# Optimization experiments

Hardware: AMD Instinct MI355X
Metric: run time of the kernel (lower is better)

## Reference

```python
import jax, jax.numpy as jnp
import numpy as np

B, D_MODEL, L = 4, 1024, 2048
HEAD_DIM = 4
H = D_MODEL // HEAD_DIM  # 256 heads of size head_dim
KD, NS, INIT_SCALE = 64, 6, 0
DECAY_MIN, DECAY_MAX = 2.0, 2.0


def _interp_linear(x, scale):
    # x: (h, Lin) -> (h, Lin*scale); matches F.interpolate(mode='linear', align_corners=False)
    if scale == 1:
        return x
    Lin = x.shape[-1]
    Lout = Lin * scale
    pos = (jnp.arange(Lout, dtype=jnp.float32) + 0.5) / scale - 0.5
    pos = jnp.clip(pos, 0.0, Lin - 1)
    lo = jnp.floor(pos).astype(jnp.int32)
    hi = jnp.minimum(lo + 1, Lin - 1)
    w = (pos - lo).astype(x.dtype)
    return x[:, lo] * (1 - w) + x[:, hi] * w


def _build_kernel(kernels, L):
    # 'cat_randn' mode: concat multi-scale interpolated kernels with decay multiplier.
    # kernels: (NS, h, KD) -> (h, L), unit-normalized per channel (norm is stop-grad,
    # mirroring the detached kernel_norm buffer initialized on first forward).
    h = kernels.shape[1]
    mult = jnp.linspace(DECAY_MIN, DECAY_MAX, h).astype(kernels.dtype)[:, None]  # (h,1)
    parts = [_interp_linear(kernels[i], 2 ** (max(0, i - 1) + INIT_SCALE)) * mult ** (NS - i - 1)
             for i in range(NS)]
    k = jnp.concatenate(parts, axis=-1)  # (h, KD*2^(NS-1))
    norm = jax.lax.stop_gradient(jnp.linalg.norm(k, axis=-1, keepdims=True))
    Lk = k.shape[-1]
    k = k[:, :L] if Lk >= L else jnp.pad(k, ((0, 0), (0, L - Lk)))
    return k / norm


def setup_inputs() -> dict:
    key = jax.random.key(0)
    ks = jax.random.split(key, 13)
    s = 0.02  # weight init scale
    return {
        'u': jax.random.normal(ks[0], (B, D_MODEL, L), jnp.float32),
        'q_w': jax.random.normal(ks[1], (D_MODEL, D_MODEL), jnp.float32) * s,
        'q_b': jax.random.normal(ks[2], (D_MODEL,), jnp.float32) * s,
        'k_w': jax.random.normal(ks[3], (D_MODEL, D_MODEL), jnp.float32) * s,
        'k_b': jax.random.normal(ks[4], (D_MODEL,), jnp.float32) * s,
        'v_w': jax.random.normal(ks[5], (D_MODEL, D_MODEL), jnp.float32) * s,
        'v_b': jax.random.normal(ks[6], (D_MODEL,), jnp.float32) * s,
        'kernels_key': jax.random.normal(ks[7], (NS, D_MODEL, KD), jnp.float32),
        'kernels': jax.random.normal(ks[8], (NS, H, KD), jnp.float32),
        'D_key': jax.random.normal(ks[9], (1, D_MODEL), jnp.float32),
        'D': jax.random.normal(ks[10], (1, H), jnp.float32),
        'pw_w': jax.random.normal(ks[11], (D_MODEL, D_MODEL), jnp.float32) * s,
        'pw_b': jax.random.normal(ks[12], (D_MODEL,), jnp.float32) * s,
    }


def reference(u, q_w, q_b, k_w, k_b, v_w, v_b, kernels_key, kernels, D_key, D, pw_w, pw_b):
    Bb, Dm, Ll = u.shape
    d = HEAD_DIM
    h = Dm // d
    n = 2 * Ll  # fft size

    k_key = _build_kernel(kernels_key, Ll)  # (Dm, L)
    k_v = _build_kernel(kernels, Ll)        # (h, L)

    # q/k/v projections (W @ u + b along channel dim)
    q = jnp.einsum('oh,bhl->bol', q_w, u) + q_b[None, :, None]
    kk = jnp.einsum('oh,bhl->bol', k_w, u) + k_b[None, :, None]
    v = jnp.einsum('oh,bhl->bol', v_w, u) + v_b[None, :, None]

    # key-side FFT long convolution + skip D_key
    key_conv = jnp.fft.irfft(jnp.fft.rfft(kk, n) * jnp.fft.rfft(k_key, n)[None], n)[..., :Ll]
    kk = key_conv + kk * D_key[0][None, :, None]

    # outer-product gating kv: (B, d1, d2, h, L)
    k_heads = kk.reshape(Bb, h, d, Ll).transpose(0, 2, 1, 3)  # (B, d1, h, L)
    v_heads = v.reshape(Bb, h, d, Ll).transpose(0, 2, 1, 3)   # (B, d2, h, L)
    kv = k_heads[:, :, None] * v_heads[:, None]               # (B, d1, d2, h, L)

    # value-side FFT long convolution + skip D
    y = jnp.fft.irfft(jnp.fft.rfft(kv, n) * jnp.fft.rfft(k_v, n)[None, None, None], n)[..., :Ll]
    y = y + kv * D[0][:, None]

    # query gating: mul_sum over d1
    q_heads = q.reshape(Bb, h, d, Ll).transpose(0, 2, 1, 3)[:, :, None]  # (B, d1, 1, h, L)
    y = (q_heads * y).sum(axis=1)                                        # (B, d2, h, L)
    y = y.reshape(Bb, Dm, Ll)

    # activation + pointwise projection, back to (B, H, L)
    y = jax.nn.gelu(jnp.transpose(y, (0, 2, 1)), approximate=False)
    y = y @ pw_w.T + pw_b
    return jnp.transpose(y, (0, 2, 1))
```

## Files before the change

### kernel.cpp

```cpp
#include <hip/hip_runtime.h>
#include <cmath>

#define B_  4
#define DM  1024
#define LL  2048
#define HH  256

#define KBSTRIDE 2120

typedef short bf16x8 __attribute__((ext_vector_type(8)));
typedef float f32x4 __attribute__((ext_vector_type(4)));

__device__ __forceinline__ float gelu_exact(float x) {
    return x * 0.5f * (1.0f + erff(x * 0.70710678118654752f));
}
__device__ __forceinline__ unsigned short f2b(float f) {
    unsigned int x = __float_as_uint(f);
    unsigned int r = x + 0x7FFFu + ((x >> 16) & 1u);
    return (unsigned short)(r >> 16);
}
__device__ __forceinline__ float b2f(unsigned short u) {
    return __uint_as_float(((unsigned int)u) << 16);
}
__device__ __forceinline__ int cvt_pk_bf16(float lo, float hi) {
    int r;
    asm("v_cvt_pk_bf16_f32 %0, %1, %2" : "=v"(r) : "v"(lo), "v"(hi));
    return r;
}

__global__ __launch_bounds__(256) void build_kernels_kernel(
        const float* __restrict__ src_key,
        const float* __restrict__ src_v,
        unsigned short* __restrict__ k_key,
        float* __restrict__ k_v) {
    int bid = blockIdx.x;
    const float* src;
    int chanstride;
    bool is_key = bid < DM;
    if (is_key) {
        src = src_key + (size_t)bid * 64;
        chanstride = DM * 64;
    } else {
        src = src_v + (size_t)(bid - DM) * 64;
        chanstride = HH * 64;
    }
    int t = threadIdx.x;
    float vals[8];
    float ss = 0.0f;
#pragma unroll
    for (int r = 0; r < 8; ++r) {
        int j = r * 256 + t;
        int i, start, scale;
        if (j < 64)        { i = 0; start = 0;    scale = 1;  }
        else if (j < 128)  { i = 1; start = 64;   scale = 1;  }
        else if (j < 256)  { i = 2; start = 128;  scale = 2;  }
        else if (j < 512)  { i = 3; start = 256;  scale = 4;  }
        else if (j < 1024) { i = 4; start = 512;  scale = 8;  }
        else               { i = 5; start = 1024; scale = 16; }
        int jj = j - start;
        float pos = ((float)jj + 0.5f) / (float)scale - 0.5f;
        pos = fminf(fmaxf(pos, 0.0f), 63.0f);
        int lo = (int)pos;
        int hi = min(lo + 1, 63);
        float w = pos - (float)lo;
        const float* s = src + (size_t)i * chanstride;
        float x0 = s[lo], x1 = s[hi];
        float mult = (float)(1 << (5 - i));
        float vv = (x0 * (1.0f - w) + x1 * w) * mult;
        vals[r] = vv;
        ss += vv * vv;
    }
#pragma unroll
    for (int off = 32; off > 0; off >>= 1) ss += __shfl_down(ss, off, 64);
    __shared__ float red[4];
    __shared__ float norm_s;
    if ((t & 63) == 0) red[t >> 6] = ss;
    __syncthreads();
    if (t == 0) norm_s = sqrtf(red[0] + red[1] + red[2] + red[3]);
    __syncthreads();
    float nrm = norm_s;
    if (is_key) {
        unsigned short* dst = k_key + (size_t)bid * LL;
#pragma unroll
        for (int r = 0; r < 8; ++r) dst[r * 256 + t] = f2b(vals[r] / nrm);
    } else {
        float* dst = k_v + (size_t)(bid - DM) * LL;
#pragma unroll
        for (int r = 0; r < 8; ++r) dst[r * 256 + t] = vals[r] / nrm;
    }
}

__global__ __launch_bounds__(256) void wcvt_kernel(
        const float* __restrict__ src, unsigned short* __restrict__ dst) {
    int i = (blockIdx.x * 256 + threadIdx.x) * 4;
    float4 x = *(const float4*)(src + i);
    ushort4 o;
    o.x = f2b(x.x); o.y = f2b(x.y); o.z = f2b(x.z); o.w = f2b(x.w);
    *(ushort4*)(dst + i) = o;
}

__global__ __launch_bounds__(256) void transpose_cvt_kernel(
        const float* __restrict__ src, unsigned short* __restrict__ dst,
        int do_gelu) {
    __shared__ float tile[64][65];
    int l0 = blockIdx.x << 6;
    int h0 = blockIdx.y << 6;
    int b  = blockIdx.z;
    int t = threadIdx.x;
    int r = t >> 4, c4 = (t & 15) << 2;
    const float* s = src + ((size_t)b * DM + h0) * LL + l0;
#pragma unroll
    for (int p = 0; p < 4; ++p) {
        float4 x = *(const float4*)(s + (size_t)(p * 16 + r) * LL + c4);
        tile[p * 16 + r][c4 + 0] = x.x;
        tile[p * 16 + r][c4 + 1] = x.y;
        tile[p * 16 + r][c4 + 2] = x.z;
        tile[p * 16 + r][c4 + 3] = x.w;
    }
    __syncthreads();
    unsigned short* d = dst + ((size_t)b * LL + l0) * DM + h0;
#pragma unroll
    for (int p = 0; p < 4; ++p) {
        int lr = p * 16 + r;
        float x0 = tile[c4 + 0][lr];
        float x1 = tile[c4 + 1][lr];
        float x2 = tile[c4 + 2][lr];
        float x3 = tile[c4 + 3][lr];
        if (do_gelu) {
            x0 = gelu_exact(x0); x1 = gelu_exact(x1);
            x2 = gelu_exact(x2); x3 = gelu_exact(x3);
        }
        ushort4 o;
        o.x = f2b(x0); o.y = f2b(x1); o.z = f2b(x2); o.w = f2b(x3);
        *(ushort4*)(d + (size_t)lr * DM + c4) = o;
    }
}

__global__ __launch_bounds__(256) void gemm_mfma_kernel(
        const unsigned short* __restrict__ A,
        const unsigned short* __restrict__ Ubf,
        const float* __restrict__ bias,
        float* __restrict__ C) {
    __shared__ unsigned short As[128 * 64];
    __shared__ unsigned short Bs[128 * 64];
    int bidx = blockIdx.x;
    int b = bidx >> 4;
    int n0 = (bidx & 15) << 7;
    int m0 = blockIdx.y << 7;
    int t = threadIdx.x;
    int lane = t & 63, wave = t >> 6;
    int wr = wave >> 1, wc = wave & 1;

    const unsigned short* Ub = Ubf + (size_t)b * LL * DM;

    f32x4 acc[4][4];
#pragma unroll
    for (int i = 0; i < 4; ++i)
#pragma unroll
        for (int j = 0; j < 4; ++j) {
            f32x4 z = {0.0f, 0.0f, 0.0f, 0.0f};
            acc[i][j] = z;
        }

    int srow = t >> 3;
    int scol = (t & 7) << 3;
    int lrow = lane & 15;
    int lk = (lane >> 4) << 3;

    for (int k0 = 0; k0 < DM; k0 += 64) {
        __syncthreads();
#pragma unroll
        for (int p = 0; p < 4; ++p) {
            int row = p * 32 + srow;
            uint4 av = *(const uint4*)(A  + (size_t)(m0 + row) * DM + k0 + scol);
            uint4 bv = *(const uint4*)(Ub + (size_t)(n0 + row) * DM + k0 + scol);
            *(uint4*)&As[row * 64 + scol] = av;
            *(uint4*)&Bs[row * 64 + scol] = bv;
        }
        __syncthreads();
#pragma unroll
        for (int kk = 0; kk < 64; kk += 32) {
            bf16x8 af[4], bfr[4];
#pragma unroll
            for (int mi = 0; mi < 4; ++mi)
                af[mi] = *(const bf16x8*)&As[(wr * 64 + mi * 16 + lrow) * 64 + kk + lk];
#pragma unroll
            for (int ni = 0; ni < 4; ++ni)
                bfr[ni] = *(const bf16x8*)&Bs[(wc * 64 + ni * 16 + lrow) * 64 + kk + lk];
#pragma unroll
            for (int mi = 0; mi < 4; ++mi)
#pragma unroll
                for (int ni = 0; ni < 4; ++ni)
                    acc[mi][ni] = __builtin_amdgcn_mfma_f32_16x16x32_bf16(
                        af[mi], bfr[ni], acc[mi][ni], 0, 0, 0);
        }
    }
    int rg = (lane >> 4) << 2;
    int cn = lane & 15;
#pragma unroll
    for (int mi = 0; mi < 4; ++mi) {
#pragma unroll
        for (int r = 0; r < 4; ++r) {
            int o = m0 + wr * 64 + mi * 16 + rg + r;
            float bo = bias[o];
            float* crow = C + ((size_t)b * DM + o) * LL + n0 + wc * 64;
#pragma unroll
            for (int ni = 0; ni < 4; ++ni)
                crow[ni * 16 + cn] = acc[mi][ni][r] + bo;
        }
    }
}

__global__ __launch_bounds__(512) void key_conv_mfma_kernel(
        const float* __restrict__ kk_raw,
        const unsigned short* __restrict__ k_key,
        const float* __restrict__ D_key,
        float* __restrict__ knew) {
    __shared__ unsigned short Kb[8 * KBSTRIDE];
    int c = blockIdx.x;
    int tid = threadIdx.x;

    const unsigned short* kp = k_key + (size_t)c * LL;
#pragma unroll
    for (int r = 0; r < 8; ++r) {
        for (int x = tid; x < 2096; x += 512) {
            int src = x + r - 48;
            Kb[r * KBSTRIDE + x] =
                (src >= 0 && src < LL) ? kp[src] : (unsigned short)0;
        }
    }
    __syncthreads();

    int w = tid >> 6, lane = tid & 63;
    int n = lane & 15, kgrp = lane >> 4;
    float zmask = (n < 4) ? 1.0f : 0.0f;
    int brow = (n < 4) ? n : 0;
    const float* pk = kk_raw + ((size_t)brow * DM + c) * LL;

    f32x4 acc[16];
#pragma unroll
    for (int m = 0; m < 16; ++m) {
        f32x4 z = {0.0f, 0.0f, 0.0f, 0.0f};
        acc[m] = z;
    }

    int idx0 = 16 * w + n + 8 * kgrp - 1999;
    int rsh = (n + 1) & 7;
    int lbase = rsh * KBSTRIDE + (idx0 - rsh);

    for (int s = 0; s < 64; ++s) {
        int t0p = s << 5;
        int tb = 2040 - t0p - 8 * kgrp;
        float4 ka = *(const float4*)(pk + tb);
        float4 kb = *(const float4*)(pk + tb + 4);
        float p0 = kb.w * zmask;
        float p1 = kb.z * zmask;
        float p2 = kb.y * zmask;
        float p3 = kb.x * zmask;
        float p4 = ka.w * zmask;
        float p5 = ka.z * zmask;
        float p6 = ka.y * zmask;
        float p7 = ka.x * zmask;
        int4 ai;
        ai.x = cvt_pk_bf16(p0, p1);
        ai.y = cvt_pk_bf16(p2, p3);
        ai.z = cvt_pk_bf16(p4, p5);
        ai.w = cvt_pk_bf16(p6, p7);
        bf16x8 afrag = __builtin_bit_cast(bf16x8, ai);

        int msv = (2128 - t0p - 16 * w) >> 7;
        msv = msv < 0 ? 0 : msv;
        int ms = __builtin_amdgcn_readfirstlane(msv);
        const unsigned short* kbp = &Kb[lbase + t0p];

#pragma unroll
        for (int m = 0; m < 16; ++m) {
            if (m >= ms) {
                bf16x8 bfrag = *(const bf16x8*)(kbp + (m << 7));
                acc[m] = __builtin_amdgcn_mfma_f32_16x16x32_bf16(
                    afrag, bfrag, acc[m], 0, 0, 0);
            }
        }
    }

    int g = lane >> 4;
    if (g == 0) {
        float dk = D_key[c];
#pragma unroll
        for (int m = 0; m < 16; ++m) {
            int lm = 16 * w + 128 * m + n;
#pragma unroll
            for (int b = 0; b < 4; ++b) {
                size_t off = ((size_t)b * DM + c) * LL + lm;
                knew[off] = acc[m][b] + kk_raw[off] * dk;
            }
        }
    }
}

__global__ __launch_bounds__(512) void value_conv_mfma_kernel(
        const float* __restrict__ knew,
        const float* __restrict__ v,
        const float* __restrict__ q,
        const float* __restrict__ k_v,
        const float* __restrict__ Dv,
        float* __restrict__ y_g) {
    __shared__ unsigned short Kb[8 * KBSTRIDE];
    int bid = blockIdx.x;
    int hh = bid & 255, b = bid >> 8;
    int tid = threadIdx.x;

    const float* kvp = k_v + (size_t)hh * LL;
#pragma unroll
    for (int r = 0; r < 8; ++r) {
        for (int x = tid; x < 2096; x += 512) {
            int src = x + r - 48;
            Kb[r * KBSTRIDE + x] =
                (src >= 0 && src < LL) ? f2b(kvp[src]) : (unsigned short)0;
        }
    }
    __syncthreads();

    int w = tid >> 6, lane = tid & 63;
    int n = lane & 15, kgrp = lane >> 4;
    int d1a = n >> 2, d2a = n & 3;

    const float* pk = knew + ((size_t)b * DM + hh * 4 + d1a) * LL;
    const float* pv = v    + ((size_t)b * DM + hh * 4 + d2a) * LL;

    f32x4 acc[16];
#pragma unroll
    for (int m = 0; m < 16; ++m) {
        f32x4 z = {0.0f, 0.0f, 0.0f, 0.0f};
        acc[m] = z;
    }

    int idx0 = 16 * w + n + 8 * kgrp - 1999;
    int rsh = (n + 1) & 7;
    int lbase = rsh * KBSTRIDE + (idx0 - rsh);

    for (int s = 0; s < 64; ++s) {
        int t0p = s << 5;
        int tb = 2040 - t0p - 8 * kgrp;
        float4 ka = *(const float4*)(pk + tb);
        float4 kb = *(const float4*)(pk + tb + 4);
        float4 va = *(const float4*)(pv + tb);
        float4 vb = *(const float4*)(pv + tb + 4);
        float p0 = kb.w * vb.w;
        float p1 = kb.z * vb.z;
        float p2 = kb.y * vb.y;
        float p3 = kb.x * vb.x;
        float p4 = ka.w * va.w;
        float p5 = ka.z * va.z;
        float p6 = ka.y * va.y;
        float p7 = ka.x * va.x;
        int4 ai;
        ai.x = cvt_pk_bf16(p0, p1);
        ai.y = cvt_pk_bf16(p2, p3);
        ai.z = cvt_pk_bf16(p4, p5);
        ai.w = cvt_pk_bf16(p6, p7);
        bf16x8 afrag = __builtin_bit_cast(bf16x8, ai);

        int msv = (2128 - t0p - 16 * w) >> 7;
        msv = msv < 0 ? 0 : msv;
        int ms = __builtin_amdgcn_readfirstlane(msv);
        const unsigned short* kbp = &Kb[lbase + t0p];

#pragma unroll
        for (int m = 0; m < 16; ++m) {
            if (m >= ms) {
                bf16x8 bfrag = *(const bf16x8*)(kbp + (m << 7));
                acc[m] = __builtin_amdgcn_mfma_f32_16x16x32_bf16(
                    afrag, bfrag, acc[m], 0, 0, 0);
            }
        }
    }

    int g = lane >> 4;
    float Dh = Dv[hh];
    const float* qrow = q    + ((size_t)b * DM + hh * 4 + g) * LL;
    const float* krow = knew + ((size_t)b * DM + hh * 4 + g) * LL;
    const float* vb0  = v    + ((size_t)b * DM + hh * 4) * LL;
#pragma unroll
    for (int m = 0; m < 16; ++m) {
        int lm = 16 * w + 128 * m + n;
        float qv = qrow[lm];
        float kl = krow[lm];
        float vl0 = vb0[lm];
        float vl1 = vb0[(size_t)1 * LL + lm];
        float vl2 = vb0[(size_t)2 * LL + lm];
        float vl3 = vb0[(size_t)3 * LL + lm];
        float part0 = qv * (acc[m][0] + kl * vl0 * Dh);
        float part1 = qv * (acc[m][1] + kl * vl1 * Dh);
        float part2 = qv * (acc[m][2] + kl * vl2 * Dh);
        float part3 = qv * (acc[m][3] + kl * vl3 * Dh);
        part0 += __shfl_xor(part0, 16, 64); part0 += __shfl_xor(part0, 32, 64);
        part1 += __shfl_xor(part1, 16, 64); part1 += __shfl_xor(part1, 32, 64);
        part2 += __shfl_xor(part2, 16, 64); part2 += __shfl_xor(part2, 32, 64);
        part3 += __shfl_xor(part3, 16, 64); part3 += __shfl_xor(part3, 32, 64);
        float outv = (g == 0) ? part0 : (g == 1) ? part1 : (g == 2) ? part2 : part3;
        y_g[((size_t)b * DM + (size_t)g * 256 + hh) * LL + lm] = outv;
    }
}

extern "C" void kernel_launch(void* const* d_in, const int* in_sizes, int n_in,
                              void* d_out, int out_size, void* d_ws, size_t ws_size,
                              hipStream_t stream) {
    const float* u       = (const float*)d_in[0];
    const float* q_w     = (const float*)d_in[1];
    const float* q_b     = (const float*)d_in[2];
    const float* k_w     = (const float*)d_in[3];
    const float* k_b     = (const float*)d_in[4];
    const float* v_w     = (const float*)d_in[5];
    const float* v_b     = (const float*)d_in[6];
    const float* kern_k  = (const float*)d_in[7];
    const float* kern_v  = (const float*)d_in[8];
    const float* D_key   = (const float*)d_in[9];
    const float* D_v     = (const float*)d_in[10];
    const float* pw_w    = (const float*)d_in[11];
    const float* pw_b    = (const float*)d_in[12];
    float* out = (float*)d_out;

    const size_t BDL = (size_t)B_ * DM * LL;
    char* p = (char*)d_ws;
    float*          w_kv   = (float*)p;          p += (size_t)HH * LL * 4;
    unsigned short* w_kkey = (unsigned short*)p; p += (size_t)DM * LL * 2;
    unsigned short* w_wbuf = (unsigned short*)p; p += (size_t)DM * DM * 2;
    float*          w_R0   = (float*)p;          p += BDL * 4;
    float*          w_q    = (float*)p;          p += BDL * 4;
    float*          w_ky   = (float*)p;          p += BDL * 4;
    float*          w_v    = (float*)p;          p += BDL * 4;
    unsigned short* w_uT   = (unsigned short*)w_R0;
    unsigned short* w_ygT  = (unsigned short*)w_R0;
    float*          w_knew = w_R0;
    float*          w_yg   = w_ky;

    build_kernels_kernel<<<DM + HH, 256, 0, stream>>>(kern_k, kern_v, w_kkey, w_kv);

    dim3 tgrid(LL / 64, DM / 64, B_);
    transpose_cvt_kernel<<<tgrid, 256, 0, stream>>>(u, w_uT, 0);

    dim3 ggrid(B_ * (LL / 128), DM / 128);
    wcvt_kernel<<<DM * DM / 1024, 256, 0, stream>>>(q_w, w_wbuf);
    gemm_mfma_kernel<<<ggrid, 256, 0, stream>>>(w_wbuf, w_uT, q_b, w_q);
    wcvt_kernel<<<DM * DM / 1024, 256, 0, stream>>>(k_w, w_wbuf);
    gemm_mfma_kernel<<<ggrid, 256, 0, stream>>>(w_wbuf, w_uT, k_b, w_ky);
    wcvt_kernel<<<DM * DM / 1024, 256, 0, stream>>>(v_w, w_wbuf);
    gemm_mfma_kernel<<<ggrid, 256, 0, stream>>>(w_wbuf, w_uT, v_b, w_v);

    key_conv_mfma_kernel<<<DM, 512, 0, stream>>>(w_ky, w_kkey, D_key, w_knew);

    value_conv_mfma_kernel<<<B_ * HH, 512, 0, stream>>>(
        w_knew, w_v, w_q, w_kv, D_v, w_yg);

    transpose_cvt_kernel<<<tgrid, 256, 0, stream>>>(w_yg, w_ygT, 1);

    wcvt_kernel<<<DM * DM / 1024, 256, 0, stream>>>(pw_w, w_wbuf);
    gemm_mfma_kernel<<<ggrid, 256, 0, stream>>>(w_wbuf, w_ygT, pw_b, out);
}
```

Before: 567.4 us.

## Reuse Toeplitz B fragments in registers across conv steps via rotating buffer

The causal-convolution MFMA loops in both conv kernels are reordered into four residue classes of the step index. Within each class, consecutive steps share 15 of their 16 shared-memory B fragments, so a 16-entry register ring buffer is filled once and then advanced by one LDS load per step instead of sixteen. Launch bounds are raised to request 2 blocks per CU. This cuts LDS read traffic, but the 16 extra bf16x8 registers on top of the 64 accumulator floats raise register pressure, which conflicts with the occupancy hint and may cause spills.

```diff
diff --git a/kernel.cpp b/kernel.cpp
--- a/kernel.cpp
+++ b/kernel.cpp
@@ -211,7 +211,7 @@
     }
 }
 
-__global__ __launch_bounds__(512) void key_conv_mfma_kernel(
+__global__ __launch_bounds__(512, 2) void key_conv_mfma_kernel(
         const float* __restrict__ kk_raw,
         const unsigned short* __restrict__ k_key,
         const float* __restrict__ D_key,
@@ -246,39 +246,55 @@
 
     int idx0 = 16 * w + n + 8 * kgrp - 1999;
     int rsh = (n + 1) & 7;
-    int lbase = rsh * KBSTRIDE + (idx0 - rsh);
-
-    for (int s = 0; s < 64; ++s) {
-        int t0p = s << 5;
-        int tb = 2040 - t0p - 8 * kgrp;
-        float4 ka = *(const float4*)(pk + tb);
-        float4 kb = *(const float4*)(pk + tb + 4);
-        float p0 = kb.w * zmask;
-        float p1 = kb.z * zmask;
-        float p2 = kb.y * zmask;
-        float p3 = kb.x * zmask;
-        float p4 = ka.w * zmask;
-        float p5 = ka.z * zmask;
-        float p6 = ka.y * zmask;
-        float p7 = ka.x * zmask;
-        int4 ai;
-        ai.x = cvt_pk_bf16(p0, p1);
-        ai.y = cvt_pk_bf16(p2, p3);
-        ai.z = cvt_pk_bf16(p4, p5);
-        ai.w = cvt_pk_bf16(p6, p7);
-        bf16x8 afrag = __builtin_bit_cast(bf16x8, ai);
-
-        int msv = (2128 - t0p - 16 * w) >> 7;
-        msv = msv < 0 ? 0 : msv;
-        int ms = __builtin_amdgcn_readfirstlane(msv);
-        const unsigned short* kbp = &Kb[lbase + t0p];
-
-#pragma unroll
-        for (int m = 0; m < 16; ++m) {
-            if (m >= ms) {
-                bf16x8 bfrag = *(const bf16x8*)(kbp + (m << 7));
-                acc[m] = __builtin_amdgcn_mfma_f32_16x16x32_bf16(
-                    afrag, bfrag, acc[m], 0, 0, 0);
+    const unsigned short* kbp = &Kb[rsh * KBSTRIDE];
+    int aoff0 = idx0 - rsh;
+
+    bf16x8 Bv[16];
+    for (int r = 0; r < 4; ++r) {
+        int off0 = aoff0 + (r << 5);
+#pragma unroll
+        for (int i = 0; i < 15; ++i) {
+            int off = off0 + (i << 7);
+            off = off < 0 ? 0 : off;
+            Bv[i] = *(const bf16x8*)(kbp + off);
+        }
+#pragma unroll
+        for (int si = 0; si < 16; ++si) {
+            {
+                int off = off0 + ((si + 15) << 7);
+                off = off < 0 ? 0 : off;
+                Bv[(si + 15) & 15] = *(const bf16x8*)(kbp + off);
+            }
+            int s = r + (si << 2);
+            int msv = (2128 - (s << 5) - 16 * w) >> 7;
+            msv = msv < 0 ? 0 : msv;
+            int ms = __builtin_amdgcn_readfirstlane(msv);
+            if (ms >= 16) continue;
+
+            int tb = 2040 - (s << 5) - 8 * kgrp;
+            float4 ka = *(const float4*)(pk + tb);
+            float4 kb = *(const float4*)(pk + tb + 4);
+            float p0 = kb.w * zmask;
+            float p1 = kb.z * zmask;
+            float p2 = kb.y * zmask;
+            float p3 = kb.x * zmask;
+            float p4 = ka.w * zmask;
+            float p5 = ka.z * zmask;
+            float p6 = ka.y * zmask;
+            float p7 = ka.x * zmask;
+            int4 ai;
+            ai.x = cvt_pk_bf16(p0, p1);
+            ai.y = cvt_pk_bf16(p2, p3);
+            ai.z = cvt_pk_bf16(p4, p5);
+            ai.w = cvt_pk_bf16(p6, p7);
+            bf16x8 afrag = __builtin_bit_cast(bf16x8, ai);
+
+#pragma unroll
+            for (int m = 0; m < 16; ++m) {
+                if (m >= ms) {
+                    acc[m] = __builtin_amdgcn_mfma_f32_16x16x32_bf16(
+                        afrag, Bv[(si + m) & 15], acc[m], 0, 0, 0);
+                }
             }
         }
     }
@@ -298,7 +314,7 @@
     }
 }
 
-__global__ __launch_bounds__(512) void value_conv_mfma_kernel(
+__global__ __launch_bounds__(512, 2) void value_conv_mfma_kernel(
         const float* __restrict__ knew,
         const float* __restrict__ v,
         const float* __restrict__ q,
@@ -337,41 +353,57 @@
 
     int idx0 = 16 * w + n + 8 * kgrp - 1999;
     int rsh = (n + 1) & 7;
-    int lbase = rsh * KBSTRIDE + (idx0 - rsh);
-
-    for (int s = 0; s < 64; ++s) {
-        int t0p = s << 5;
-        int tb = 2040 - t0p - 8 * kgrp;
-        float4 ka = *(const float4*)(pk + tb);
-        float4 kb = *(const float4*)(pk + tb + 4);
-        float4 va = *(const float4*)(pv + tb);
-        float4 vb = *(const float4*)(pv + tb + 4);
-        float p0 = kb.w * vb.w;
-        float p1 = kb.z * vb.z;
-        float p2 = kb.y * vb.y;
-        float p3 = kb.x * vb.x;
-        float p4 = ka.w * va.w;
-        float p5 = ka.z * va.z;
-        float p6 = ka.y * va.y;
-        float p7 = ka.x * va.x;
-        int4 ai;
-        ai.x = cvt_pk_bf16(p0, p1);
-        ai.y = cvt_pk_bf16(p2, p3);
-        ai.z = cvt_pk_bf16(p4, p5);
-        ai.w = cvt_pk_bf16(p6, p7);
-        bf16x8 afrag = __builtin_bit_cast(bf16x8, ai);
-
-        int msv = (2128 - t0p - 16 * w) >> 7;
-        msv = msv < 0 ? 0 : msv;
-        int ms = __builtin_amdgcn_readfirstlane(msv);
-        const unsigned short* kbp = &Kb[lbase + t0p];
-
-#pragma unroll
-        for (int m = 0; m < 16; ++m) {
-            if (m >= ms) {
-                bf16x8 bfrag = *(const bf16x8*)(kbp + (m << 7));
-                acc[m] = __builtin_amdgcn_mfma_f32_16x16x32_bf16(
-                    afrag, bfrag, acc[m], 0, 0, 0);
+    const unsigned short* kbp = &Kb[rsh * KBSTRIDE];
+    int aoff0 = idx0 - rsh;
+
+    bf16x8 Bv[16];
+    for (int r = 0; r < 4; ++r) {
+        int off0 = aoff0 + (r << 5);
+#pragma unroll
+        for (int i = 0; i < 15; ++i) {
+            int off = off0 + (i << 7);
+            off = off < 0 ? 0 : off;
+            Bv[i] = *(const bf16x8*)(kbp + off);
+        }
+#pragma unroll
+        for (int si = 0; si < 16; ++si) {
+            {
+                int off = off0 + ((si + 15) << 7);
+                off = off < 0 ? 0 : off;
+                Bv[(si + 15) & 15] = *(const bf16x8*)(kbp + off);
+            }
+            int s = r + (si << 2);
+            int msv = (2128 - (s << 5) - 16 * w) >> 7;
+            msv = msv < 0 ? 0 : msv;
+            int ms = __builtin_amdgcn_readfirstlane(msv);
+            if (ms >= 16) continue;
+
+            int tb = 2040 - (s << 5) - 8 * kgrp;
+            float4 ka = *(const float4*)(pk + tb);
+            float4 kb = *(const float4*)(pk + tb + 4);
+            float4 va = *(const float4*)(pv + tb);
+            float4 vb = *(const float4*)(pv + tb + 4);
+            float p0 = kb.w * vb.w;
+            float p1 = kb.z * vb.z;
+            float p2 = kb.y * vb.y;
+            float p3 = kb.x * vb.x;
+            float p4 = ka.w * va.w;
+            float p5 = ka.z * va.z;
+            float p6 = ka.y * va.y;
+            float p7 = ka.x * va.x;
+            int4 ai;
+            ai.x = cvt_pk_bf16(p0, p1);
+            ai.y = cvt_pk_bf16(p2, p3);
+            ai.z = cvt_pk_bf16(p4, p5);
+            ai.w = cvt_pk_bf16(p6, p7);
+            bf16x8 afrag = __builtin_bit_cast(bf16x8, ai);
+
+#pragma unroll
+            for (int m = 0; m < 16; ++m) {
+                if (m >= ms) {
+                    acc[m] = __builtin_amdgcn_mfma_f32_16x16x32_bf16(
+                        afrag, Bv[(si + m) & 15], acc[m], 0, 0, 0);
+                }
             }
         }
     }
```

Measured after the change: 611.8 us. 1.08x slower.
